# Kernel optimization log

Hardware: AMD Instinct MI355X
Metric: run time of the kernel (lower is better)

## Reference

```python
import jax, jax.numpy as jnp
import numpy as np


def setup_inputs() -> dict:
    key = jax.random.key(0)
    ks = jax.random.split(key, 6)
    B, L, D, H, W = 32, 1024, 128, 128, 9
    F = D + W  # feature dim after one-hot positional embed
    rn = lambda k, shape, s: (jax.random.normal(k, shape, jnp.float32) * s)
    return {
        "embeddings": rn(ks[0], (B, L, D), 1.0),
        "masks": jnp.ones((B, L), jnp.float32),  # unused in math (as in source)
        "w1_w": rn(ks[1], (F, H), 0.05),
        "w1_b": jnp.zeros((H,), jnp.float32),
        "w2_w": rn(ks[2], (F, H), 0.05),
        "w2_b": jnp.zeros((H,), jnp.float32),
        "v_w": rn(ks[3], (H, 1), 0.05),
        "v_b": jnp.zeros((1,), jnp.float32),
        "cnn_w": rn(ks[4], (F * W, H), 0.02),
        "cnn_b": jnp.zeros((H,), jnp.float32),
        "window_size": 9,
    }


def reference(embeddings, masks, w1_w, w1_b, w2_w, w2_b, v_w, v_b, cnn_w, cnn_b, window_size):
    # Vectorized form of the per-position loop in LocalConvolutionLayer.forward.
    B, L, D = embeddings.shape
    W = window_size
    half = W // 2
    # Zero-pad then gather all sliding windows at once: [B, L, W, D]
    padded = jnp.pad(embeddings, ((0, 0), (half, half), (0, 0)))
    idx = jnp.arange(L)[:, None] + jnp.arange(W)[None, :]  # [L, W]
    win = padded[:, idx, :]
    # One-hot within-window positional embedding, concatenated on channels -> F = D + W
    pos = jnp.broadcast_to(jnp.eye(W, dtype=embeddings.dtype), (B, L, W, W))
    ctx = jnp.concatenate([win, pos], axis=-1)  # [B, L, W, F]
    ent = ctx[:, :, half, :]                    # center token, [B, L, F]
    # AttentionLayer: v(tanh(w1(ent)[:,None] + w2(ctx)))
    re = ent @ w1_w + w1_b                      # [B, L, H]
    rc = ctx @ w2_w + w2_b                      # [B, L, W, H]
    scores = jnp.tanh(re[:, :, None, :] + rc) @ v_w + v_b  # [B, L, W, 1]
    weights = jax.nn.softmax(scores, axis=2)
    out = (weights * ctx).reshape(B, L, W * ctx.shape[-1])  # [B, L, W*F]
    return out @ cnn_w + cnn_b                  # [B, L, H]
```

## Files before the change

### kernel.cpp

```cpp
#include <hip/hip_runtime.h>
#include <hip/hip_bf16.h>


typedef __attribute__((ext_vector_type(8))) short bf16x8;
typedef __attribute__((ext_vector_type(4))) float f32x4;

#define LL 1024
#define TANHK 2.885390081777927f

__device__ __forceinline__ unsigned short f2bf(float f) {
  unsigned int u = __float_as_uint(f);
  u = u + 0x7FFFu + ((u >> 16) & 1u);
  return (unsigned short)(u >> 16);
}
__device__ __forceinline__ float bf2f(unsigned short us) {
  return __uint_as_float(((unsigned int)us) << 16);
}

__global__ __launch_bounds__(256) void prep_kernel(
    const float* __restrict__ w1, const float* __restrict__ w2,
    const float* __restrict__ cnn,
    unsigned short* __restrict__ W12Bt, unsigned short* __restrict__ CwBt) {
  int gid = blockIdx.x * 256 + threadIdx.x;
  if (blockIdx.x < 128) {
    int n = gid >> 7, d = gid & 127;
    float v = (n < 128) ? w1[d * 128 + n] : w2[d * 128 + (n - 128)];
    W12Bt[n * 128 + d] = f2bf(v);
  } else {
    int idx = gid - 32768;
    int h = idx / 1152;
    int c = idx - h * 1152;
    int w = c >> 7, d = c & 127;
    CwBt[h * 1152 + c] = f2bf(cnn[(w * 137 + d) * 128 + h]);
  }
}

__global__ __launch_bounds__(512, 4) void mega_kernel(
    const float* __restrict__ emb,
    const unsigned short* __restrict__ W12Bt,
    const unsigned short* __restrict__ CwBt,
    const float* __restrict__ w1, const float* __restrict__ w1b,
    const float* __restrict__ w2, const float* __restrict__ w2b,
    const float* __restrict__ vw,
    const float* __restrict__ cnn, const float* __restrict__ cnnb,
    float* __restrict__ out) {
  extern __shared__ __align__(16) unsigned char smem[];
  uint4* E            = (uint4*)smem;
  unsigned short* Hs  = (unsigned short*)(smem + 20480);
  float* pwL          = (float*)(smem + 61440);
  float* vwL          = (float*)(smem + 66048);
  float* wtT          = (float*)(smem + 66560);

  int tid = threadIdx.x;
  int bid = blockIdx.x;
  int b = bid >> 4, l0 = (bid & 15) << 6;
  int lane = tid & 63, wid = tid >> 6;
  int l15 = lane & 15, l4 = lane >> 4;

  #pragma unroll
  for (int s = 0; s < 5; ++s) {
    int i = tid + s * 512;
    if (i < 1280) {
      int er = i >> 4, g = i & 15;
      int t = l0 + er - 4;
      uint4 v = {0u, 0u, 0u, 0u};
      if (er < 72 && t >= 0 && t < LL) {
        const float4* src = (const float4*)(emb + ((size_t)(b * LL + t) << 7) + g * 8);
        float4 x0 = src[0], x1 = src[1];
        v.x = f2bf(x0.x) | ((unsigned)f2bf(x0.y) << 16);
        v.y = f2bf(x0.z) | ((unsigned)f2bf(x0.w) << 16);
        v.z = f2bf(x1.x) | ((unsigned)f2bf(x1.y) << 16);
        v.w = f2bf(x1.z) | ((unsigned)f2bf(x1.w) << 16);
      }
      E[er * 16 + (g ^ (er & 7))] = v;
    } else if (i < 2432) {
      int idx = i - 1280;
      int w = idx >> 7, h = idx & 127;
      pwL[idx] = TANHK * (w2[(128 + w) * 128 + h] + w2b[h] +
                          w1[132 * 128 + h] + w1b[h]);
    } else {
      int h = i - 2432;
      vwL[h] = vw[h];
    }
  }
  __syncthreads();

  const bf16x8* Eb = (const bf16x8*)E;
  #pragma unroll
  for (int jj = 0; jj < 2; ++jj) {
    int job = wid + jj * 8;
    if (job < 10) {
      int part = job >= 5;
      int er0 = (job - part * 5) * 16;
      f32x4 acc[8];
      #pragma unroll
      for (int nn = 0; nn < 8; ++nn) acc[nn] = (f32x4){0.f, 0.f, 0.f, 0.f};
      #pragma unroll
      for (int kk = 0; kk < 4; ++kk) {
        int gk = kk * 4 + l4;
        int er = er0 + l15;
        bf16x8 aF = Eb[er * 16 + (gk ^ (er & 7))];
        #pragma unroll
        for (int nn = 0; nn < 8; ++nn) {
          bf16x8 bF = *(const bf16x8*)(W12Bt +
              (size_t)((part << 7) + nn * 16 + l15) * 128 + gk * 8);
          acc[nn] = __builtin_amdgcn_mfma_f32_16x16x32_bf16(aF, bF, acc[nn], 0, 0, 0);
        }
      }
      unsigned short* Hp = Hs + part * 10240;
      #pragma unroll
      for (int nn = 0; nn < 8; ++nn)
        #pragma unroll
        for (int j = 0; j < 4; ++j) {
          int i2 = er0 + l4 * 4 + j;
          Hp[i2 * 128 + ((nn * 16 + l15) ^ (l4 << 4))] = f2bf(TANHK * acc[nn][j]);
        }
    }
  }
  __syncthreads();

  {
    int q = lane >> 4, u = lane & 15, u8 = u * 8;
    const unsigned short* Hs1 = Hs;
    const unsigned short* Hs2 = Hs + 10240;
    #pragma unroll
    for (int pass = 0; pass < 2; ++pass) {
      int r = wid * 8 + pass * 4 + q;
      int fi = r + 4;
      int fxor = ((fi >> 2) & 3) << 4;
      bf16x8 fraw = *(const bf16x8*)&Hs1[fi * 128 + (u8 ^ fxor)];
      float fr[8];
      #pragma unroll
      for (int j = 0; j < 8; ++j) fr[j] = bf2f((unsigned short)fraw[j]);
      f32x4 vr0 = *(const f32x4*)&vwL[u8];
      f32x4 vr1 = *(const f32x4*)&vwL[u8 + 4];
      float sc[9];
      #pragma unroll
      for (int w = 0; w < 9; ++w) {
        int gi = r + w;
        int gxor = ((gi >> 2) & 3) << 4;
        bf16x8 graw = *(const bf16x8*)&Hs2[gi * 128 + (u8 ^ gxor)];
        f32x4 pw0 = *(const f32x4*)&pwL[w * 128 + u8];
        f32x4 pw1 = *(const f32x4*)&pwL[w * 128 + u8 + 4];
        float a = 0.f;
        #pragma unroll
        for (int j = 0; j < 4; ++j) {
          float e = exp2f(fr[j] + bf2f((unsigned short)graw[j]) + pw0[j]);
          a = fmaf(vr0[j], __builtin_amdgcn_rcpf(1.f + e), a);
        }
        #pragma unroll
        for (int j = 0; j < 4; ++j) {
          float e = exp2f(fr[4 + j] + bf2f((unsigned short)graw[4 + j]) + pw1[j]);
          a = fmaf(vr1[j], __builtin_amdgcn_rcpf(1.f + e), a);
        }
        a += __shfl_xor(a, 1, 64);
        a += __shfl_xor(a, 2, 64);
        a += __shfl_xor(a, 4, 64);
        a += __shfl_xor(a, 8, 64);
        sc[w] = a;
      }
      float mn = sc[0];
      #pragma unroll
      for (int w = 1; w < 9; ++w) mn = fminf(mn, sc[w]);
      float p[9], sum = 0.f;
      #pragma unroll
      for (int w = 0; w < 9; ++w) { p[w] = exp2f(TANHK * (mn - sc[w])); sum += p[w]; }
      float inv = __builtin_amdgcn_rcpf(sum);
      if (u < 9) {
        float wv = p[0];
        #pragma unroll
        for (int w = 1; w < 9; ++w) wv = (u == w) ? p[w] : wv;
        wtT[u * 68 + r] = wv * inv;
      }
    }
  }
  __syncthreads();

  int wr = wid >> 2, wc = wid & 3;
  int h0 = wc * 32 + l15;
  f32x4 fin[2][2];
  #pragma unroll
  for (int m = 0; m < 2; ++m)
    #pragma unroll
    for (int n = 0; n < 2; ++n) fin[m][n] = (f32x4){0.f, 0.f, 0.f, 0.f};
  #pragma unroll
  for (int w = 0; w < 9; ++w) {
    f32x4 tmp[2][2];
    #pragma unroll
    for (int m = 0; m < 2; ++m)
      #pragma unroll
      for (int n = 0; n < 2; ++n) tmp[m][n] = (f32x4){0.f, 0.f, 0.f, 0.f};
    #pragma unroll
    for (int kk = 0; kk < 4; ++kk) {
      int gk = kk * 4 + l4;
      bf16x8 aF[2];
      #pragma unroll
      for (int m = 0; m < 2; ++m) {
        int er = wr * 32 + m * 16 + l15 + w;
        aF[m] = Eb[er * 16 + (gk ^ (er & 7))];
      }
      #pragma unroll
      for (int n = 0; n < 2; ++n) {
        int hh = wc * 32 + n * 16 + l15;
        bf16x8 bF = *(const bf16x8*)(CwBt + (size_t)hh * 1152 + w * 128 + gk * 8);
        #pragma unroll
        for (int m = 0; m < 2; ++m)
          tmp[m][n] = __builtin_amdgcn_mfma_f32_16x16x32_bf16(aF[m], bF, tmp[m][n], 0, 0, 0);
      }
    }
    float cp0 = cnn[(w * 138 + 128) * 128 + h0];
    float cp1 = cnn[(w * 138 + 128) * 128 + h0 + 16];
    #pragma unroll
    for (int m = 0; m < 2; ++m) {
      f32x4 wt4 = *(const f32x4*)&wtT[w * 68 + wr * 32 + m * 16 + l4 * 4];
      #pragma unroll
      for (int j = 0; j < 4; ++j) {
        fin[m][0][j] += wt4[j] * (tmp[m][0][j] + cp0);
        fin[m][1][j] += wt4[j] * (tmp[m][1][j] + cp1);
      }
    }
  }
  float cb0 = cnnb[h0], cb1 = cnnb[h0 + 16];
  #pragma unroll
  for (int m = 0; m < 2; ++m)
    #pragma unroll
    for (int j = 0; j < 4; ++j) {
      int r = wr * 32 + m * 16 + l4 * 4 + j;
      size_t o = ((size_t)(b * LL + l0 + r) << 7) + h0;
      out[o]      = fin[m][0][j] + cb0;
      out[o + 16] = fin[m][1][j] + cb1;
    }
}

extern "C" void kernel_launch(void* const* d_in, const int* in_sizes, int n_in,
                              void* d_out, int out_size, void* d_ws, size_t ws_size,
                              hipStream_t stream) {
  const float* emb  = (const float*)d_in[0];
  const float* w1   = (const float*)d_in[2];
  const float* w1b  = (const float*)d_in[3];
  const float* w2   = (const float*)d_in[4];
  const float* w2b  = (const float*)d_in[5];
  const float* vw   = (const float*)d_in[6];
  const float* cnn  = (const float*)d_in[8];
  const float* cnnb = (const float*)d_in[9];
  float* out = (float*)d_out;

  char* ws = (char*)d_ws;
  unsigned short* W12Bt = (unsigned short*)(ws);
  unsigned short* CwBt  = (unsigned short*)(ws + 65536);

  prep_kernel<<<704, 256, 0, stream>>>(w1, w2, cnn, W12Bt, CwBt);
  mega_kernel<<<512, 512, 69008, stream>>>(emb, W12Bt, CwBt, w1, w1b, w2, w2b,
                                           vw, cnn, cnnb, out);
}
```

Measured before the change: 153.7 us.

## Pre-swizzle weights into MFMA fragment order and trim projection jobs

The prep kernel now writes W1/W2 and CNN weights in per-lane MFMA fragment order, so each lane's B-operand load in the main kernel is a contiguous, fully coalesced 16-byte read instead of a strided gather. The H projection job split also changes: W1 is now computed only for the 64 center rows instead of 80, giving 9 jobs instead of 10, and the LDS xor swizzle is adjusted to match the new row offsets. This cuts global load transactions and some redundant MFMA work, at the cost of a more intricate index mapping that must stay consistent.

```diff
diff --git a/kernel.cpp b/kernel.cpp
--- a/kernel.cpp
+++ b/kernel.cpp
@@ -20,25 +20,30 @@
 __global__ __launch_bounds__(256) void prep_kernel(
     const float* __restrict__ w1, const float* __restrict__ w2,
     const float* __restrict__ cnn,
-    unsigned short* __restrict__ W12Bt, unsigned short* __restrict__ CwBt) {
+    unsigned short* __restrict__ W12Frag, unsigned short* __restrict__ CwFrag) {
   int gid = blockIdx.x * 256 + threadIdx.x;
   if (blockIdx.x < 128) {
-    int n = gid >> 7, d = gid & 127;
+    int d = gid >> 8, n = gid & 255;
     float v = (n < 128) ? w1[d * 128 + n] : w2[d * 128 + (n - 128)];
-    W12Bt[n * 128 + d] = f2bf(v);
+    int tile = (n >> 4) * 4 + (d >> 5);
+    int lane = ((d >> 3) & 3) * 16 + (n & 15);
+    W12Frag[(tile * 64 + lane) * 8 + (d & 7)] = f2bf(v);
   } else {
     int idx = gid - 32768;
-    int h = idx / 1152;
-    int c = idx - h * 1152;
-    int w = c >> 7, d = c & 127;
-    CwBt[h * 1152 + c] = f2bf(cnn[(w * 137 + d) * 128 + h]);
+    int h = idx & 127;
+    int wd = idx >> 7;
+    int w = wd >> 7, d = wd & 127;
+    float v = cnn[(w * 137 + d) * 128 + h];
+    int tile = (w * 8 + (h >> 4)) * 4 + (d >> 5);
+    int lane = ((d >> 3) & 3) * 16 + (h & 15);
+    CwFrag[(tile * 64 + lane) * 8 + (d & 7)] = f2bf(v);
   }
 }
 
 __global__ __launch_bounds__(512, 4) void mega_kernel(
     const float* __restrict__ emb,
-    const unsigned short* __restrict__ W12Bt,
-    const unsigned short* __restrict__ CwBt,
+    const unsigned short* __restrict__ W12Frag,
+    const unsigned short* __restrict__ CwFrag,
     const float* __restrict__ w1, const float* __restrict__ w1b,
     const float* __restrict__ w2, const float* __restrict__ w2b,
     const float* __restrict__ vw,
@@ -56,6 +61,8 @@
   int b = bid >> 4, l0 = (bid & 15) << 6;
   int lane = tid & 63, wid = tid >> 6;
   int l15 = lane & 15, l4 = lane >> 4;
+  const bf16x8* Wf = (const bf16x8*)W12Frag;
+  const bf16x8* Cf = (const bf16x8*)CwFrag;
 
   #pragma unroll
   for (int s = 0; s < 5; ++s) {
@@ -87,11 +94,11 @@
 
   const bf16x8* Eb = (const bf16x8*)E;
   #pragma unroll
-  for (int jj = 0; jj < 2; ++jj) {
-    int job = wid + jj * 8;
-    if (job < 10) {
-      int part = job >= 5;
-      int er0 = (job - part * 5) * 16;
+  for (int it = 0; it < 2; ++it) {
+    int job = it == 0 ? wid : 8;
+    if (it == 0 || wid == 0) {
+      int part = job >= 4;
+      int er0 = part ? (job - 4) * 16 : 4 + job * 16;
       f32x4 acc[8];
       #pragma unroll
       for (int nn = 0; nn < 8; ++nn) acc[nn] = (f32x4){0.f, 0.f, 0.f, 0.f};
@@ -102,18 +109,18 @@
         bf16x8 aF = Eb[er * 16 + (gk ^ (er & 7))];
         #pragma unroll
         for (int nn = 0; nn < 8; ++nn) {
-          bf16x8 bF = *(const bf16x8*)(W12Bt +
-              (size_t)((part << 7) + nn * 16 + l15) * 128 + gk * 8);
+          bf16x8 bF = Wf[((part * 8 + nn) * 4 + kk) * 64 + lane];
           acc[nn] = __builtin_amdgcn_mfma_f32_16x16x32_bf16(aF, bF, acc[nn], 0, 0, 0);
         }
       }
       unsigned short* Hp = Hs + part * 10240;
+      int hxor = (((er0 >> 2) + l4) & 3) << 4;
       #pragma unroll
       for (int nn = 0; nn < 8; ++nn)
         #pragma unroll
         for (int j = 0; j < 4; ++j) {
           int i2 = er0 + l4 * 4 + j;
-          Hp[i2 * 128 + ((nn * 16 + l15) ^ (l4 << 4))] = f2bf(TANHK * acc[nn][j]);
+          Hp[i2 * 128 + ((nn * 16 + l15) ^ hxor)] = f2bf(TANHK * acc[nn][j]);
         }
     }
   }
@@ -201,8 +208,7 @@
       }
       #pragma unroll
       for (int n = 0; n < 2; ++n) {
-        int hh = wc * 32 + n * 16 + l15;
-        bf16x8 bF = *(const bf16x8*)(CwBt + (size_t)hh * 1152 + w * 128 + gk * 8);
+        bf16x8 bF = Cf[((w * 8 + wc * 2 + n) * 4 + kk) * 64 + lane];
         #pragma unroll
         for (int m = 0; m < 2; ++m)
           tmp[m][n] = __builtin_amdgcn_mfma_f32_16x16x32_bf16(aF[m], bF, tmp[m][n], 0, 0, 0);
@@ -246,10 +252,10 @@
   float* out = (float*)d_out;
 
   char* ws = (char*)d_ws;
-  unsigned short* W12Bt = (unsigned short*)(ws);
-  unsigned short* CwBt  = (unsigned short*)(ws + 65536);
-
-  prep_kernel<<<704, 256, 0, stream>>>(w1, w2, cnn, W12Bt, CwBt);
-  mega_kernel<<<512, 512, 69008, stream>>>(emb, W12Bt, CwBt, w1, w1b, w2, w2b,
+  unsigned short* W12Frag = (unsigned short*)(ws);
+  unsigned short* CwFrag  = (unsigned short*)(ws + 65536);
+
+  prep_kernel<<<704, 256, 0, stream>>>(w1, w2, cnn, W12Frag, CwFrag);
+  mega_kernel<<<512, 512, 69008, stream>>>(emb, W12Frag, CwFrag, w1, w1b, w2, w2b,
                                            vw, cnn, cnnb, out);
 }
```

Measured after the change: 130.8 us. -14.9%, faster.
